# Kernel optimization log

Hardware: AMD Instinct MI355X
Metric: run time of the kernel (lower is better)

## Reference

```python
import jax, jax.numpy as jnp
import numpy as np

N_NODES = 50000
N_EDGES = 800000
IN_DIM = 128
HID = 32
HEADS = 4


def _lin_init(key, fan_in, fan_out):
    k1, k2 = jax.random.split(key)
    s = 1.0 / np.sqrt(fan_in)
    W = jax.random.uniform(k1, (fan_in, fan_out), jnp.float32, -s, s)
    b = jax.random.uniform(k2, (fan_out,), jnp.float32, -s, s)
    return W, b


def setup_inputs() -> dict:
    key = jax.random.key(0)
    keys = jax.random.split(key, 12)
    x = jax.random.normal(keys[0], (N_NODES, IN_DIM), jnp.float32)
    edge_index = jax.random.randint(keys[1], (2, N_EDGES), 0, N_NODES, jnp.int64)

    # conv1: in_dim -> heads*hid (128 -> 4*32)
    Wq1, bq1 = _lin_init(keys[2], IN_DIM, HEADS * HID)
    Wk1, bk1 = _lin_init(keys[3], IN_DIM, HEADS * HID)
    Wv1, bv1 = _lin_init(keys[4], IN_DIM, HEADS * HID)
    Ws1, bs1 = _lin_init(keys[5], IN_DIM, HEADS * HID)
    # conv2: 128 -> 1*32
    Wq2, bq2 = _lin_init(keys[6], HEADS * HID, HID)
    Wk2, bk2 = _lin_init(keys[7], HEADS * HID, HID)
    Wv2, bv2 = _lin_init(keys[8], HEADS * HID, HID)
    Ws2, bs2 = _lin_init(keys[9], HEADS * HID, HID)
    # output linear: 32 -> 1
    Wo, bo = _lin_init(keys[10], HID, 1)

    return {
        "x": x, "edge_index": edge_index,
        "Wq1": Wq1, "bq1": bq1, "Wk1": Wk1, "bk1": bk1,
        "Wv1": Wv1, "bv1": bv1, "Ws1": Ws1, "bs1": bs1,
        "Wq2": Wq2, "bq2": bq2, "Wk2": Wk2, "bk2": bk2,
        "Wv2": Wv2, "bv2": bv2, "Ws2": Ws2, "bs2": bs2,
        "Wo": Wo, "bo": bo,
    }


def transformer_conv(x, edge_index, Wq, bq, Wk, bk, Wv, bv, Ws, bs, heads, d):
    # PyG TransformerConv (concat=True, root_weight=True, beta=False, no edge attr).
    n = x.shape[0]
    src, dst = edge_index[0], edge_index[1]  # message j(src) -> i(dst)
    q = (x @ Wq + bq).reshape(n, heads, d)
    k = (x @ Wk + bk).reshape(n, heads, d)
    v = (x @ Wv + bv).reshape(n, heads, d)
    # per-edge attention logits [E, heads]
    logits = (q[dst] * k[src]).sum(-1) / jnp.sqrt(jnp.float32(d))
    # segment softmax over incoming edges of each target node
    m = jax.ops.segment_max(logits, dst, num_segments=n)
    p = jnp.exp(logits - m[dst])
    denom = jax.ops.segment_sum(p, dst, num_segments=n)
    alpha = p / denom[dst]  # [E, heads]
    # weighted scatter-add of values
    msg = alpha[:, :, None] * v[src]  # [E, heads, d]
    aggr = jax.ops.segment_sum(msg, dst, num_segments=n).reshape(n, heads * d)
    return aggr + x @ Ws + bs  # root (skip) connection


def reference(x, edge_index,
              Wq1, bq1, Wk1, bk1, Wv1, bv1, Ws1, bs1,
              Wq2, bq2, Wk2, bk2, Wv2, bv2, Ws2, bs2,
              Wo, bo):
    h = transformer_conv(x, edge_index, Wq1, bq1, Wk1, bk1, Wv1, bv1, Ws1, bs1, HEADS, HID)
    h = jax.nn.relu(h)
    h = transformer_conv(h, edge_index, Wq2, bq2, Wk2, bk2, Wv2, bv2, Ws2, bs2, 1, HID)
    h = jax.nn.relu(h)
    g = h.mean(axis=0)  # [HID]
    return g @ Wo + bo  # [1]
```

## Files before the change

kernel.cpp:

```cpp
#include <hip/hip_runtime.h>
#include <math.h>

#define N_NODES 50000
#define N_EDGES 800000
#define NBK 196
#define BCAP 6144

typedef short short8 __attribute__((ext_vector_type(8)));
typedef float f32x4 __attribute__((ext_vector_type(4)));
typedef float f32x2 __attribute__((ext_vector_type(2)));

__device__ inline unsigned short f2bf(float v) {
  unsigned u = __float_as_uint(v);
  u += 0x7FFFu + ((u >> 16) & 1u);
  return (unsigned short)(u >> 16);
}
__device__ inline float bf2f(unsigned short b) {
  return __uint_as_float(((unsigned)b) << 16);
}
__device__ inline float bflo(unsigned u) { return __uint_as_float(u << 16); }
__device__ inline float bfhi(unsigned u) { return __uint_as_float(u & 0xFFFF0000u); }
__device__ inline unsigned char f2fp8(float v) {
  return (unsigned char)(__builtin_amdgcn_cvt_pk_fp8_f32(v, 0.f, 0, false) & 0xFF);
}
template <bool HI>
__device__ inline f32x2 fp8dec(unsigned u) {
  return __builtin_amdgcn_cvt_pk_f32_fp8(u, HI);
}

#define SCL 0.17677669529663687f

#define W1_B 256
#define W2_B 64
__global__ void prep_fused(const float* __restrict__ Wq1, const float* __restrict__ Wk1,
                           const float* __restrict__ Wv1, const float* __restrict__ Ws1,
                           const float* __restrict__ bq1, const float* __restrict__ bk1,
                           const float* __restrict__ bv1, const float* __restrict__ bs1,
                           const float* __restrict__ Wq2, const float* __restrict__ Wk2,
                           const float* __restrict__ Wv2, const float* __restrict__ Ws2,
                           const float* __restrict__ bq2, const float* __restrict__ bk2,
                           const float* __restrict__ bv2, const float* __restrict__ bs2,
                           unsigned short* __restrict__ Wt1, float* __restrict__ bcat1,
                           unsigned short* __restrict__ Wt2, float* __restrict__ bcat2,
                           const int* __restrict__ ei, int* __restrict__ bhist, int E) {
  const int b = blockIdx.x, tid = threadIdx.x;
  if (b < W1_B) {
    int i = b * 256 + tid;
    int c = i >> 7, k = i & 127;
    int mi = c >> 7, lc = c & 127;
    const float* W = (mi == 0) ? Wq1 : (mi == 1) ? Wk1 : (mi == 2) ? Wv1 : Ws1;
    float scl = (mi == 0) ? SCL : 1.f;
    Wt1[i] = f2bf(W[(size_t)k * 128 + lc] * scl);
    if (i < 512) {
      int bm = i >> 7, bl = i & 127;
      const float* bb = (bm == 0) ? bq1 : (bm == 1) ? bk1 : (bm == 2) ? bv1 : bs1;
      bcat1[i] = bb[bl] * ((bm == 0) ? SCL : 1.f);
    }
  } else if (b < W1_B + W2_B) {
    int i = (b - W1_B) * 256 + tid;
    int c = i >> 7, k = i & 127;
    int mi = c >> 5, lc = c & 31;
    const float* W = (mi == 0) ? Wq2 : (mi == 1) ? Wk2 : (mi == 2) ? Wv2 : Ws2;
    float scl = (mi == 0) ? SCL : 1.f;
    Wt2[i] = f2bf(W[(size_t)k * 32 + lc] * scl);
    if (i < 128) {
      int bm = i >> 5, bl = i & 31;
      const float* bb = (bm == 0) ? bq2 : (bm == 1) ? bk2 : (bm == 2) ? bv2 : bs2;
      bcat2[i] = bb[bl] * ((bm == 0) ? SCL : 1.f);
    }
  } else {
    __shared__ int h[NBK];
    for (int i = tid; i < NBK; i += 256) h[i] = 0;
    __syncthreads();
    int e = (b - W1_B - W2_B) * 4096 + tid;
#pragma unroll
    for (int p = 0; p < 16; ++p, e += 256)
      if (e < E) atomicAdd(&h[ei[E + e] >> 8], 1);
    __syncthreads();
    for (int i = tid; i < NBK; i += 256)
      if (h[i]) atomicAdd(&bhist[i], h[i]);
  }
}

__global__ __launch_bounds__(256) void gemm_conv1(
    const float* __restrict__ X, const unsigned short* __restrict__ Wt,
    const float* __restrict__ bcat, unsigned short* __restrict__ Q1b,
    unsigned short* __restrict__ SK1, unsigned char* __restrict__ KV8, int M) {
  __shared__ __align__(16) unsigned char L[3][64 * 272];
  unsigned short* As = (unsigned short*)L[0];
  const int bm = blockIdx.x * 64;
  const int tid = threadIdx.x, wave = tid >> 6, lane = tid & 63;
  const int lr = lane & 15, q = lane >> 4;

#pragma unroll
  for (int p = 0; p < 8; ++p) {
    int f = tid + p * 256;
    int row = f >> 5, c4 = f & 31;
    int gm = bm + row; if (gm >= M) gm = 0;
    float4 v = *(const float4*)(X + (size_t)gm * 128 + c4 * 4);
    ushort4 o;
    o.x = f2bf(v.x); o.y = f2bf(v.y); o.z = f2bf(v.z); o.w = f2bf(v.w);
    *(ushort4*)&As[row * 136 + c4 * 4] = o;
  }
  __syncthreads();

  const int colbase = wave * 128;
  f32x4 acc[4][8];
#pragma unroll
  for (int i = 0; i < 4; ++i)
#pragma unroll
    for (int j = 0; j < 8; ++j) acc[i][j] = (f32x4){0.f, 0.f, 0.f, 0.f};

#pragma unroll
  for (int ks = 0; ks < 4; ++ks) {
    short8 af[4];
#pragma unroll
    for (int i = 0; i < 4; ++i)
      af[i] = *(short8*)&As[(i * 16 + lr) * 136 + ks * 32 + q * 8];
#pragma unroll
    for (int j = 0; j < 8; ++j) {
      short8 bf = *(const short8*)(Wt + (size_t)(colbase + j * 16 + lr) * 128 + ks * 32 + q * 8);
#pragma unroll
      for (int i = 0; i < 4; ++i)
        acc[i][j] = __builtin_amdgcn_mfma_f32_16x16x32_bf16(af[i], bf, acc[i][j], 0, 0, 0);
    }
  }
  __syncthreads();

  float bj[8];
#pragma unroll
  for (int j = 0; j < 8; ++j) bj[j] = bcat[colbase + j * 16 + lr];

  if (wave == 0 || wave == 3) {
    unsigned short* Ls16 = (unsigned short*)((wave == 0) ? L[1] : L[0]);
#pragma unroll
    for (int i = 0; i < 4; ++i)
#pragma unroll
      for (int r = 0; r < 4; ++r) {
        int row = i * 16 + q * 4 + r;
#pragma unroll
        for (int j = 0; j < 8; ++j)
          Ls16[row * 136 + j * 16 + lr] = f2bf(acc[i][j][r] + bj[j]);
      }
  } else {
    unsigned char* KLs = L[2];
    const int voff = (wave == 2) ? 2 : 0;
#pragma unroll
    for (int i = 0; i < 4; ++i)
#pragma unroll
      for (int r = 0; r < 4; ++r) {
        int row = i * 16 + q * 4 + r;
#pragma unroll
        for (int j = 0; j < 8; ++j) {
          int d = j * 16 + lr;
          KLs[row * 272 + 4 * (d >> 1) + voff + (d & 1)] = f2fp8(acc[i][j][r] + bj[j]);
        }
      }
  }
  __syncthreads();

#pragma unroll
  for (int p = 0; p < 4; ++p) {
    int f = tid + p * 256;
    int row = f >> 4, u = f & 15;
    int gr = bm + row;
    if (gr < M) {
      *(uint4*)(Q1b + (size_t)gr * 128 + u * 8) = *(uint4*)&((unsigned short*)L[1])[row * 136 + u * 8];
      *(uint4*)(KV8 + (size_t)gr * 256 + u * 16) = *(uint4*)&L[2][row * 272 + u * 16];
      *(uint4*)(SK1 + (size_t)gr * 128 + u * 8) = *(uint4*)&((unsigned short*)L[0])[row * 136 + u * 8];
    }
  }
}

__global__ __launch_bounds__(256) void gemm2(
    const unsigned short* __restrict__ Ab, const unsigned short* __restrict__ Wt,
    const float* __restrict__ bcat, unsigned char* __restrict__ C2b, int M) {
  __shared__ __align__(16) unsigned short As[64 * 136];
  __shared__ __align__(16) unsigned char Lsb[64 * 272];
  const int bm = blockIdx.x * 64;
  const int tid = threadIdx.x, wave = tid >> 6, lane = tid & 63;
  const int lr = lane & 15, q = lane >> 4;

#pragma unroll
  for (int p = 0; p < 4; ++p) {
    int f = tid + p * 256;
    int row = f >> 4, chunk = f & 15;
    int gm = bm + row; if (gm >= M) gm = 0;
    uint4 v = *(const uint4*)(Ab + (size_t)gm * 128 + chunk * 8);
    *(uint4*)&As[row * 136 + chunk * 8] = v;
  }
  __syncthreads();

  f32x4 acc[4][2];
#pragma unroll
  for (int i = 0; i < 4; ++i)
#pragma unroll
    for (int j = 0; j < 2; ++j) acc[i][j] = (f32x4){0.f, 0.f, 0.f, 0.f};

#pragma unroll
  for (int ks = 0; ks < 4; ++ks) {
    short8 af[4];
#pragma unroll
    for (int i = 0; i < 4; ++i)
      af[i] = *(short8*)&As[(i * 16 + lr) * 136 + ks * 32 + q * 8];
#pragma unroll
    for (int j = 0; j < 2; ++j) {
      short8 bf = *(const short8*)(Wt + (size_t)(wave * 32 + j * 16 + lr) * 128 + ks * 32 + q * 8);
#pragma unroll
      for (int i = 0; i < 4; ++i)
        acc[i][j] = __builtin_amdgcn_mfma_f32_16x16x32_bf16(af[i], bf, acc[i][j], 0, 0, 0);
    }
  }

  float bj[2];
#pragma unroll
  for (int j = 0; j < 2; ++j) bj[j] = bcat[wave * 32 + j * 16 + lr];
#pragma unroll
  for (int i = 0; i < 4; ++i)
#pragma unroll
    for (int r = 0; r < 4; ++r) {
      int row = i * 16 + q * 4 + r;
#pragma unroll
      for (int j = 0; j < 2; ++j) {
        int c = wave * 32 + j * 16 + lr;
        float val = acc[i][j][r] + bj[j];
        if (c < 32) {
          *(unsigned short*)&Lsb[row * 272 + 2 * c] = f2bf(val);
        } else if (c < 64) {
          int d = c - 32;
          Lsb[row * 272 + 64 + 4 * (d >> 1) + (d & 1)] = f2fp8(val);
        } else if (c < 96) {
          int d = c - 64;
          Lsb[row * 272 + 64 + 4 * (d >> 1) + 2 + (d & 1)] = f2fp8(val);
        } else {
          *(unsigned short*)&Lsb[row * 272 + 192 + 2 * (c - 96)] = f2bf(val);
        }
      }
    }
  __syncthreads();
#pragma unroll
  for (int p = 0; p < 16; ++p) {
    int idx = tid + p * 256;
    int row = idx >> 6, u = idx & 63;
    int gr = bm + row;
    if (gr < M) *(unsigned*)(C2b + (size_t)gr * 256 + u * 4) = *(const unsigned*)&Lsb[row * 272 + u * 4];
  }
}

__global__ void bucket_scan(const int* __restrict__ bhist, int* __restrict__ boff,
                            int* __restrict__ bcur) {
  __shared__ int s[256];
  int t = threadIdx.x;
  int v = (t < NBK) ? bhist[t] : 0;
  s[t] = v;
  __syncthreads();
#pragma unroll
  for (int off = 1; off < 256; off <<= 1) {
    int u = (t >= off) ? s[t - off] : 0;
    __syncthreads();
    s[t] += u;
    __syncthreads();
  }
  if (t < NBK) {
    int excl = s[t] - v;
    boff[t] = excl;
    bcur[t] = excl;
  }
  if (t == NBK - 1) boff[NBK] = s[t];
}

__global__ void bucket_scatter(const int* __restrict__ ei, int* __restrict__ bcur,
                               int* __restrict__ ebuck, int E) {
  __shared__ int lh[NBK];
  for (int i = threadIdx.x; i < NBK; i += 256) lh[i] = 0;
  __syncthreads();
  const int e0 = blockIdx.x * 4096;
  int pks[16], bks[16];
#pragma unroll
  for (int p = 0; p < 16; ++p) {
    int e = e0 + p * 256 + threadIdx.x;
    if (e < E) {
      int src = ei[e], dst = ei[E + e];
      pks[p] = (src << 8) | (dst & 255);
      bks[p] = dst >> 8;
      atomicAdd(&lh[bks[p]], 1);
    } else bks[p] = -1;
  }
  __syncthreads();
  for (int i = threadIdx.x; i < NBK; i += 256)
    if (lh[i]) lh[i] = atomicAdd(&bcur[i], lh[i]);
  __syncthreads();
#pragma unroll
  for (int p = 0; p < 16; ++p) {
    if (bks[p] >= 0) {
      int slot = atomicAdd(&lh[bks[p]], 1);
      ebuck[slot] = pks[p];
    }
  }
}

__global__ void bucket_csr(const int* __restrict__ ebuck, const int* __restrict__ boff,
                           int* __restrict__ rowptr, int* __restrict__ esrc, int N) {
  const int b = blockIdx.x;
  const int lo = boff[b], hi = boff[b + 1];
  const int cnt = hi - lo;
  __shared__ int hist[256];
  __shared__ int cur[256];
  __shared__ int sorted[BCAP];
  const int t = threadIdx.x;
  hist[t] = 0;
  __syncthreads();
  for (int i = t; i < cnt; i += 256) atomicAdd(&hist[ebuck[lo + i] & 255], 1);
  __syncthreads();
  int v = hist[t];
  sorted[t] = v;
  __syncthreads();
#pragma unroll
  for (int off = 1; off < 256; off <<= 1) {
    int u = (t >= off) ? sorted[t - off] : 0;
    __syncthreads();
    sorted[t] += u;
    __syncthreads();
  }
  int excl = sorted[t] - v;
  cur[t] = excl;
  int node = b * 256 + t;
  if (node <= N) rowptr[node] = lo + excl;
  __syncthreads();
  for (int i = t; i < cnt; i += 256) {
    int pk = ebuck[lo + i];
    int slot = atomicAdd(&cur[pk & 255], 1);
    if (slot < BCAP) sorted[slot] = pk;
    else esrc[lo + slot] = pk & 0xFFFFFF00;
  }
  __syncthreads();
  int lim = cnt < BCAP ? cnt : BCAP;
  for (int i = t; i < lim; i += 256) esrc[lo + i] = sorted[i] & 0xFFFFFF00;
}

__global__ void node_attn1(const int* __restrict__ rowptr, const int* __restrict__ esrc,
                           const unsigned short* __restrict__ Qb,
                           const unsigned char* __restrict__ KV8,
                           const unsigned short* __restrict__ SK, unsigned short* __restrict__ Hb,
                           int n) {
  int node = (blockIdx.x * blockDim.x + threadIdx.x) >> 6;
  int lane = threadIdx.x & 63;
  if (node >= n) return;
  const int half = lane >> 5, ll = lane & 31;
  const int r0 = rowptr[node], r1 = rowptr[node + 1];
  uint2 qq = *(const uint2*)(Qb + (size_t)node * 128 + ll * 4);
  const float q0 = bflo(qq.x), q1 = bfhi(qq.x), q2 = bflo(qq.y), q3 = bfhi(qq.y);
  float l = 0.f, a0 = 0.f, a1 = 0.f, a2 = 0.f, a3 = 0.f;
  const unsigned char* kvb = KV8 + ll * 8;
  int j = r0;
  for (; j + 8 <= r1; j += 8) {
    int e = j + half * 4;
    int s0 = esrc[e], s1 = esrc[e + 1], s2 = esrc[e + 2], s3 = esrc[e + 3];
    uint2 u0 = *(const uint2*)(kvb + s0);
    uint2 u1 = *(const uint2*)(kvb + s1);
    uint2 u2 = *(const uint2*)(kvb + s2);
    uint2 u3 = *(const uint2*)(kvb + s3);
    f32x2 k0a = fp8dec<false>(u0.x), k0b = fp8dec<false>(u0.y);
    f32x2 k1a = fp8dec<false>(u1.x), k1b = fp8dec<false>(u1.y);
    f32x2 k2a = fp8dec<false>(u2.x), k2b = fp8dec<false>(u2.y);
    f32x2 k3a = fp8dec<false>(u3.x), k3b = fp8dec<false>(u3.y);
    float d0 = q0 * k0a.x + q1 * k0a.y + q2 * k0b.x + q3 * k0b.y;
    float d1 = q0 * k1a.x + q1 * k1a.y + q2 * k1b.x + q3 * k1b.y;
    float d2 = q0 * k2a.x + q1 * k2a.y + q2 * k2b.x + q3 * k2b.y;
    float d3 = q0 * k3a.x + q1 * k3a.y + q2 * k3b.x + q3 * k3b.y;
#pragma unroll
    for (int msk = 1; msk <= 4; msk <<= 1) {
      d0 += __shfl_xor(d0, msk);
      d1 += __shfl_xor(d1, msk);
      d2 += __shfl_xor(d2, msk);
      d3 += __shfl_xor(d3, msk);
    }
    float p0 = __expf(d0), p1 = __expf(d1), p2 = __expf(d2), p3 = __expf(d3);
    l += (p0 + p1) + (p2 + p3);
    f32x2 v0a = fp8dec<true>(u0.x), v0b = fp8dec<true>(u0.y);
    f32x2 v1a = fp8dec<true>(u1.x), v1b = fp8dec<true>(u1.y);
    f32x2 v2a = fp8dec<true>(u2.x), v2b = fp8dec<true>(u2.y);
    f32x2 v3a = fp8dec<true>(u3.x), v3b = fp8dec<true>(u3.y);
    a0 += p0 * v0a.x + p1 * v1a.x + p2 * v2a.x + p3 * v3a.x;
    a1 += p0 * v0a.y + p1 * v1a.y + p2 * v2a.y + p3 * v3a.y;
    a2 += p0 * v0b.x + p1 * v1b.x + p2 * v2b.x + p3 * v3b.x;
    a3 += p0 * v0b.y + p1 * v1b.y + p2 * v2b.y + p3 * v3b.y;
  }
  for (; j < r1; j += 4) {
    int eA = j + half * 2, eB = eA + 1;
    bool vA = eA < r1, vB = eB < r1;
    int sA = esrc[vA ? eA : r0];
    int sB = esrc[vB ? eB : r0];
    uint2 ua = *(const uint2*)(kvb + sA);
    uint2 ub = *(const uint2*)(kvb + sB);
    f32x2 ka1 = fp8dec<false>(ua.x), ka2 = fp8dec<false>(ua.y);
    f32x2 kb1 = fp8dec<false>(ub.x), kb2 = fp8dec<false>(ub.y);
    float dA = q0 * ka1.x + q1 * ka1.y + q2 * ka2.x + q3 * ka2.y;
    float dB = q0 * kb1.x + q1 * kb1.y + q2 * kb2.x + q3 * kb2.y;
#pragma unroll
    for (int msk = 1; msk <= 4; msk <<= 1) {
      dA += __shfl_xor(dA, msk);
      dB += __shfl_xor(dB, msk);
    }
    float pA = vA ? __expf(dA) : 0.f;
    float pB = vB ? __expf(dB) : 0.f;
    l += pA + pB;
    f32x2 va1 = fp8dec<true>(ua.x), va2 = fp8dec<true>(ua.y);
    f32x2 vb1 = fp8dec<true>(ub.x), vb2 = fp8dec<true>(ub.y);
    a0 += pA * va1.x + pB * vb1.x;
    a1 += pA * va1.y + pB * vb1.y;
    a2 += pA * va2.x + pB * vb2.x;
    a3 += pA * va2.y + pB * vb2.y;
  }
  l  += __shfl_xor(l, 32);
  a0 += __shfl_xor(a0, 32);
  a1 += __shfl_xor(a1, 32);
  a2 += __shfl_xor(a2, 32);
  a3 += __shfl_xor(a3, 32);
  float inv = (l > 0.f) ? 1.f / l : 0.f;
  if (half == 0) {
    uint2 sk = *(const uint2*)(SK + (size_t)node * 128 + ll * 4);
    float o0 = fmaxf(bflo(sk.x) + a0 * inv, 0.f);
    float o1 = fmaxf(bfhi(sk.x) + a1 * inv, 0.f);
    float o2 = fmaxf(bflo(sk.y) + a2 * inv, 0.f);
    float o3 = fmaxf(bfhi(sk.y) + a3 * inv, 0.f);
    uint2 hb;
    hb.x = ((unsigned)f2bf(o1) << 16) | (unsigned)f2bf(o0);
    hb.y = ((unsigned)f2bf(o3) << 16) | (unsigned)f2bf(o2);
    *(uint2*)(Hb + (size_t)node * 128 + ll * 4) = hb;
  }
}

__global__ void node_attn2(const int* __restrict__ rowptr, const int* __restrict__ esrc,
                           unsigned char* __restrict__ C2b, int n) {
  int node = (blockIdx.x * blockDim.x + threadIdx.x) >> 6;
  int lane = threadIdx.x & 63;
  if (node >= n) return;
  const int g = lane >> 4, gl = lane & 15;
  const int r0 = rowptr[node], r1 = rowptr[node + 1];
  unsigned qu = *(const unsigned*)(C2b + (size_t)node * 256 + gl * 4);
  const float q0 = bflo(qu), q1 = bfhi(qu);
  float l = 0.f, a0 = 0.f, a1 = 0.f;
  const unsigned char* kvb = C2b + 64 + gl * 4;
  int j = r0;
  for (; j + 8 <= r1; j += 8) {
    int e = j + g * 2;
    int s0 = esrc[e], s1 = esrc[e + 1];
    unsigned u0 = *(const unsigned*)(kvb + s0);
    unsigned u1 = *(const unsigned*)(kvb + s1);
    f32x2 k0 = fp8dec<false>(u0), k1 = fp8dec<false>(u1);
    float d0 = q0 * k0.x + q1 * k0.y;
    float d1 = q0 * k1.x + q1 * k1.y;
#pragma unroll
    for (int msk = 1; msk <= 8; msk <<= 1) {
      d0 += __shfl_xor(d0, msk);
      d1 += __shfl_xor(d1, msk);
    }
    float p0 = __expf(d0), p1 = __expf(d1);
    l += p0 + p1;
    f32x2 v0 = fp8dec<true>(u0), v1 = fp8dec<true>(u1);
    a0 += p0 * v0.x + p1 * v1.x;
    a1 += p0 * v0.y + p1 * v1.y;
  }
  for (; j < r1; j += 4) {
    bool v = (j + g) < r1;
    int s = esrc[v ? j + g : r0];
    unsigned u = *(const unsigned*)(kvb + s);
    f32x2 kd = fp8dec<false>(u);
    float d = q0 * kd.x + q1 * kd.y;
#pragma unroll
    for (int msk = 1; msk <= 8; msk <<= 1) d += __shfl_xor(d, msk);
    float p = v ? __expf(d) : 0.f;
    l += p;
    f32x2 vd = fp8dec<true>(u);
    a0 += p * vd.x;
    a1 += p * vd.y;
  }
#pragma unroll
  for (int msk = 16; msk <= 32; msk <<= 1) {
    l  += __shfl_xor(l, msk);
    a0 += __shfl_xor(a0, msk);
    a1 += __shfl_xor(a1, msk);
  }
  float inv = (l > 0.f) ? 1.f / l : 0.f;
  if (lane < 16) {
    unsigned* h = (unsigned*)(C2b + (size_t)node * 256 + 192 + gl * 4);
    unsigned hu = *h;
    float o0 = bflo(hu) + a0 * inv;
    float o1 = bfhi(hu) + a1 * inv;
    *h = ((unsigned)f2bf(o1) << 16) | (unsigned)f2bf(o0);
  }
}

__global__ void mean_reduce(const unsigned char* __restrict__ C2b, float* __restrict__ ACC, int n) {
  __shared__ float s[256];
  float acc = 0.f;
  int stride = gridDim.x * blockDim.x;
  int total = n * 32;
  for (int i = blockIdx.x * blockDim.x + threadIdx.x; i < total; i += stride) {
    int node = i >> 5, c = i & 31;
    unsigned short h = *(const unsigned short*)(C2b + (size_t)node * 256 + 192 + c * 2);
    acc += fmaxf(bf2f(h), 0.f);
  }
  s[threadIdx.x] = acc;
  __syncthreads();
  for (int off = 128; off >= 32; off >>= 1) {
    if (threadIdx.x < off) s[threadIdx.x] += s[threadIdx.x + off];
    __syncthreads();
  }
  if (threadIdx.x < 32) atomicAdd(&ACC[threadIdx.x], s[threadIdx.x]);
}

__global__ void final_out(const float* __restrict__ ACC, const float* __restrict__ Wo,
                          const float* __restrict__ bo, float* __restrict__ out, float invN) {
  int lane = threadIdx.x;
  float v = 0.f;
  if (lane < 32) v = ACC[lane] * invN * Wo[lane];
  v += __shfl_xor(v, 1);
  v += __shfl_xor(v, 2);
  v += __shfl_xor(v, 4);
  v += __shfl_xor(v, 8);
  v += __shfl_xor(v, 16);
  v += __shfl_xor(v, 32);
  if (lane == 0) out[0] = v + bo[0];
}

extern "C" void kernel_launch(void* const* d_in, const int* in_sizes, int n_in,
                              void* d_out, int out_size, void* d_ws, size_t ws_size,
                              hipStream_t stream) {
  const float* x   = (const float*)d_in[0];
  const int*   ei  = (const int*)d_in[1];
  const float* Wq1 = (const float*)d_in[2];  const float* bq1 = (const float*)d_in[3];
  const float* Wk1 = (const float*)d_in[4];  const float* bk1 = (const float*)d_in[5];
  const float* Wv1 = (const float*)d_in[6];  const float* bv1 = (const float*)d_in[7];
  const float* Ws1 = (const float*)d_in[8];  const float* bs1 = (const float*)d_in[9];
  const float* Wq2 = (const float*)d_in[10]; const float* bq2 = (const float*)d_in[11];
  const float* Wk2 = (const float*)d_in[12]; const float* bk2 = (const float*)d_in[13];
  const float* Wv2 = (const float*)d_in[14]; const float* bv2 = (const float*)d_in[15];
  const float* Ws2 = (const float*)d_in[16]; const float* bs2 = (const float*)d_in[17];
  const float* Wo  = (const float*)d_in[18]; const float* bo  = (const float*)d_in[19];

  char* ws = (char*)d_ws;
  const int N = N_NODES, E = N_EDGES;
  const int GB = (N + 63) / 64;
  const int EB = (E + 4095) / 4096;

  unsigned short* Q1b = (unsigned short*)(ws + 0);
  unsigned short* SK1 = (unsigned short*)(ws + 12800000);
  unsigned char*  KV1 = (unsigned char*)(ws + 25600000);
  unsigned short* H1b = (unsigned short*)(ws + 51200000);
  unsigned char*  C2  = (unsigned char*)(ws + 64000000);
  int* rowptr = (int*)(ws + 89600000);
  int* esrc   = (int*)(ws + 89900032);
  int* bhist  = (int*)(ws + 93100032);
  int* boff   = (int*)(ws + 93101056);
  int* bcur   = (int*)(ws + 93102080);
  unsigned short* Wt1   = (unsigned short*)(ws + 93103104);
  unsigned short* Wt2   = (unsigned short*)(ws + 93234176);
  float*          bcat1 = (float*)(ws + 93266944);
  float*          bcat2 = (float*)(ws + 93268992);
  float*          ACC   = (float*)(ws + 93269504);
  int*            ebuck = (int*)(ws + 93270016);

  float* out = (float*)d_out;

  dim3 blk(256);

  hipMemsetAsync(bhist, 0, NBK * sizeof(int), stream);
  hipMemsetAsync(ACC, 0, 32 * sizeof(float), stream);

  prep_fused<<<dim3(W1_B + W2_B + EB), blk, 0, stream>>>(
      Wq1, Wk1, Wv1, Ws1, bq1, bk1, bv1, bs1,
      Wq2, Wk2, Wv2, Ws2, bq2, bk2, bv2, bs2,
      Wt1, bcat1, Wt2, bcat2, ei, bhist, E);

  bucket_scan<<<dim3(1), blk, 0, stream>>>(bhist, boff, bcur);
  bucket_scatter<<<dim3(EB), blk, 0, stream>>>(ei, bcur, ebuck, E);
  bucket_csr<<<dim3(NBK), blk, 0, stream>>>(ebuck, boff, rowptr, esrc, N);

  gemm_conv1<<<dim3(GB), blk, 0, stream>>>(x, Wt1, bcat1, Q1b, SK1, KV1, N);

  node_attn1<<<dim3((N * 64 + 255) / 256), blk, 0, stream>>>(rowptr, esrc, Q1b, KV1, SK1, H1b, N);

  gemm2<<<dim3(GB), blk, 0, stream>>>(H1b, Wt2, bcat2, C2, N);

  node_attn2<<<dim3((N * 64 + 255) / 256), blk, 0, stream>>>(rowptr, esrc, C2, N);

  mean_reduce<<<dim3(1024), blk, 0, stream>>>(C2, ACC, N);
  final_out<<<dim3(1), dim3(64), 0, stream>>>(ACC, Wo, bo, out, 1.0f / (float)N);
}
```

Measured before the change: 270.0 us.

## Fuse edge bucket scatter into conv1 GEMM and fold mean/output into attn2

The bucket scatter blocks become a prefix of the conv1 GEMM launch, so edge bucketing and the first projection share one grid instead of running back to back. node_attn2 now applies ReLU, dots with Wo and writes one partial sum per block. A single-block final_out reduces these partials, which removes the mean_reduce kernel, the ACC memset, the global atomics and the write-back of h2. The cost is a larger fused kernel whose scatter blocks hold the same large shared-memory footprint as the GEMM blocks.

```diff
diff --git a/kernel.cpp b/kernel.cpp
--- a/kernel.cpp
+++ b/kernel.cpp
@@ -82,14 +82,69 @@
   }
 }
 
-__global__ __launch_bounds__(256) void gemm_conv1(
+__global__ void bucket_scan(const int* __restrict__ bhist, int* __restrict__ boff,
+                            int* __restrict__ bcur) {
+  __shared__ int s[256];
+  int t = threadIdx.x;
+  int v = (t < NBK) ? bhist[t] : 0;
+  s[t] = v;
+  __syncthreads();
+#pragma unroll
+  for (int off = 1; off < 256; off <<= 1) {
+    int u = (t >= off) ? s[t - off] : 0;
+    __syncthreads();
+    s[t] += u;
+    __syncthreads();
+  }
+  if (t < NBK) {
+    int excl = s[t] - v;
+    boff[t] = excl;
+    bcur[t] = excl;
+  }
+  if (t == NBK - 1) boff[NBK] = s[t];
+}
+
+__global__ __launch_bounds__(256) void scatter_gemm1(
+    const int* __restrict__ ei, int* __restrict__ bcur, int* __restrict__ ebuck, int E, int EB,
     const float* __restrict__ X, const unsigned short* __restrict__ Wt,
     const float* __restrict__ bcat, unsigned short* __restrict__ Q1b,
     unsigned short* __restrict__ SK1, unsigned char* __restrict__ KV8, int M) {
   __shared__ __align__(16) unsigned char L[3][64 * 272];
+  const int tid = threadIdx.x;
+
+  if ((int)blockIdx.x < EB) {
+    int* lh = (int*)L[0];
+    for (int i = tid; i < NBK; i += 256) lh[i] = 0;
+    __syncthreads();
+    const int e0 = blockIdx.x * 4096;
+    int pks[16], bks[16];
+#pragma unroll
+    for (int p = 0; p < 16; ++p) {
+      int e = e0 + p * 256 + tid;
+      if (e < E) {
+        int src = ei[e], dst = ei[E + e];
+        pks[p] = (src << 8) | (dst & 255);
+        bks[p] = dst >> 8;
+        atomicAdd(&lh[bks[p]], 1);
+      } else bks[p] = -1;
+    }
+    __syncthreads();
+    for (int i = tid; i < NBK; i += 256)
+      if (lh[i]) lh[i] = atomicAdd(&bcur[i], lh[i]);
+    __syncthreads();
+#pragma unroll
+    for (int p = 0; p < 16; ++p) {
+      if (bks[p] >= 0) {
+        int slot = atomicAdd(&lh[bks[p]], 1);
+        ebuck[slot] = pks[p];
+      }
+    }
+    return;
+  }
+
   unsigned short* As = (unsigned short*)L[0];
-  const int bm = blockIdx.x * 64;
-  const int tid = threadIdx.x, wave = tid >> 6, lane = tid & 63;
+  const int bm = (blockIdx.x - EB) * 64;
+  const int wave = tid >> 6, lane = tid & 63;
   const int lr = lane & 15, q = lane >> 4;
 
 #pragma unroll
@@ -170,6 +225,45 @@
       *(uint4*)(SK1 + (size_t)gr * 128 + u * 8) = *(uint4*)&((unsigned short*)L[0])[row * 136 + u * 8];
     }
   }
+}
+
+__global__ void bucket_csr(const int* __restrict__ ebuck, const int* __restrict__ boff,
+                           int* __restrict__ rowptr, int* __restrict__ esrc, int N) {
+  const int b = blockIdx.x;
+  const int lo = boff[b], hi = boff[b + 1];
+  const int cnt = hi - lo;
+  __shared__ int hist[256];
+  __shared__ int cur[256];
+  __shared__ int sorted[BCAP];
+  const int t = threadIdx.x;
+  hist[t] = 0;
+  __syncthreads();
+  for (int i = t; i < cnt; i += 256) atomicAdd(&hist[ebuck[lo + i] & 255], 1);
+  __syncthreads();
+  int v = hist[t];
+  sorted[t] = v;
+  __syncthreads();
+#pragma unroll
+  for (int off = 1; off < 256; off <<= 1) {
+    int u = (t >= off) ? sorted[t - off] : 0;
+    __syncthreads();
+    sorted[t] += u;
+    __syncthreads();
+  }
+  int excl = sorted[t] - v;
+  cur[t] = excl;
+  int node = b * 256 + t;
+  if (node <= N) rowptr[node] = lo + excl;
+  __syncthreads();
+  for (int i = t; i < cnt; i += 256) {
+    int pk = ebuck[lo + i];
+    int slot = atomicAdd(&cur[pk & 255], 1);
+    if (slot < BCAP) sorted[slot] = pk;
+    else esrc[lo + slot] = pk & 0xFFFFFF00;
+  }
+  __syncthreads();
+  int lim = cnt < BCAP ? cnt : BCAP;
+  for (int i = t; i < lim; i += 256) esrc[lo + i] = sorted[i] & 0xFFFFFF00;
 }
 
 __global__ __launch_bounds__(256) void gemm2(
@@ -245,97 +339,6 @@
     int gr = bm + row;
     if (gr < M) *(unsigned*)(C2b + (size_t)gr * 256 + u * 4) = *(const unsigned*)&Lsb[row * 272 + u * 4];
   }
-}
-
-__global__ void bucket_scan(const int* __restrict__ bhist, int* __restrict__ boff,
-                            int* __restrict__ bcur) {
-  __shared__ int s[256];
-  int t = threadIdx.x;
-  int v = (t < NBK) ? bhist[t] : 0;
-  s[t] = v;
-  __syncthreads();
-#pragma unroll
-  for (int off = 1; off < 256; off <<= 1) {
-    int u = (t >= off) ? s[t - off] : 0;
-    __syncthreads();
-    s[t] += u;
-    __syncthreads();
-  }
-  if (t < NBK) {
-    int excl = s[t] - v;
-    boff[t] = excl;
-    bcur[t] = excl;
-  }
-  if (t == NBK - 1) boff[NBK] = s[t];
-}
-
-__global__ void bucket_scatter(const int* __restrict__ ei, int* __restrict__ bcur,
-                               int* __restrict__ ebuck, int E) {
-  __shared__ int lh[NBK];
-  for (int i = threadIdx.x; i < NBK; i += 256) lh[i] = 0;
-  __syncthreads();
-  const int e0 = blockIdx.x * 4096;
-  int pks[16], bks[16];
-#pragma unroll
-  for (int p = 0; p < 16; ++p) {
-    int e = e0 + p * 256 + threadIdx.x;
-    if (e < E) {
-      int src = ei[e], dst = ei[E + e];
-      pks[p] = (src << 8) | (dst & 255);
-      bks[p] = dst >> 8;
-      atomicAdd(&lh[bks[p]], 1);
-    } else bks[p] = -1;
-  }
-  __syncthreads();
-  for (int i = threadIdx.x; i < NBK; i += 256)
-    if (lh[i]) lh[i] = atomicAdd(&bcur[i], lh[i]);
-  __syncthreads();
-#pragma unroll
-  for (int p = 0; p < 16; ++p) {
-    if (bks[p] >= 0) {
-      int slot = atomicAdd(&lh[bks[p]], 1);
-      ebuck[slot] = pks[p];
-    }
-  }
-}
-
-__global__ void bucket_csr(const int* __restrict__ ebuck, const int* __restrict__ boff,
-                           int* __restrict__ rowptr, int* __restrict__ esrc, int N) {
-  const int b = blockIdx.x;
-  const int lo = boff[b], hi = boff[b + 1];
-  const int cnt = hi - lo;
-  __shared__ int hist[256];
-  __shared__ int cur[256];
-  __shared__ int sorted[BCAP];
-  const int t = threadIdx.x;
-  hist[t] = 0;
-  __syncthreads();
-  for (int i = t; i < cnt; i += 256) atomicAdd(&hist[ebuck[lo + i] & 255], 1);
-  __syncthreads();
-  int v = hist[t];
-  sorted[t] = v;
-  __syncthreads();
-#pragma unroll
-  for (int off = 1; off < 256; off <<= 1) {
-    int u = (t >= off) ? sorted[t - off] : 0;
-    __syncthreads();
-    sorted[t] += u;
-    __syncthreads();
-  }
-  int excl = sorted[t] - v;
-  cur[t] = excl;
-  int node = b * 256 + t;
-  if (node <= N) rowptr[node] = lo + excl;
-  __syncthreads();
-  for (int i = t; i < cnt; i += 256) {
-    int pk = ebuck[lo + i];
-    int slot = atomicAdd(&cur[pk & 255], 1);
-    if (slot < BCAP) sorted[slot] = pk;
-    else esrc[lo + slot] = pk & 0xFFFFFF00;
-  }
-  __syncthreads();
-  int lim = cnt < BCAP ? cnt : BCAP;
-  for (int i = t; i < lim; i += 256) esrc[lo + i] = sorted[i] & 0xFFFFFF00;
 }
 
 __global__ void node_attn1(const int* __restrict__ rowptr, const int* __restrict__ esrc,
@@ -432,97 +435,85 @@
 }
 
 __global__ void node_attn2(const int* __restrict__ rowptr, const int* __restrict__ esrc,
-                           unsigned char* __restrict__ C2b, int n) {
+                           const unsigned char* __restrict__ C2b, const float* __restrict__ Wo,
+                           float* __restrict__ pblock, int n) {
+  __shared__ float ps[4];
   int node = (blockIdx.x * blockDim.x + threadIdx.x) >> 6;
   int lane = threadIdx.x & 63;
-  if (node >= n) return;
+  int wave = threadIdx.x >> 6;
   const int g = lane >> 4, gl = lane & 15;
-  const int r0 = rowptr[node], r1 = rowptr[node + 1];
-  unsigned qu = *(const unsigned*)(C2b + (size_t)node * 256 + gl * 4);
-  const float q0 = bflo(qu), q1 = bfhi(qu);
-  float l = 0.f, a0 = 0.f, a1 = 0.f;
-  const unsigned char* kvb = C2b + 64 + gl * 4;
-  int j = r0;
-  for (; j + 8 <= r1; j += 8) {
-    int e = j + g * 2;
-    int s0 = esrc[e], s1 = esrc[e + 1];
-    unsigned u0 = *(const unsigned*)(kvb + s0);
-    unsigned u1 = *(const unsigned*)(kvb + s1);
-    f32x2 k0 = fp8dec<false>(u0), k1 = fp8dec<false>(u1);
-    float d0 = q0 * k0.x + q1 * k0.y;
-    float d1 = q0 * k1.x + q1 * k1.y;
-#pragma unroll
-    for (int msk = 1; msk <= 8; msk <<= 1) {
-      d0 += __shfl_xor(d0, msk);
-      d1 += __shfl_xor(d1, msk);
-    }
-    float p0 = __expf(d0), p1 = __expf(d1);
-    l += p0 + p1;
-    f32x2 v0 = fp8dec<true>(u0), v1 = fp8dec<true>(u1);
-    a0 += p0 * v0.x + p1 * v1.x;
-    a1 += p0 * v0.y + p1 * v1.y;
-  }
-  for (; j < r1; j += 4) {
-    bool v = (j + g) < r1;
-    int s = esrc[v ? j + g : r0];
-    unsigned u = *(const unsigned*)(kvb + s);
-    f32x2 kd = fp8dec<false>(u);
-    float d = q0 * kd.x + q1 * kd.y;
-#pragma unroll
-    for (int msk = 1; msk <= 8; msk <<= 1) d += __shfl_xor(d, msk);
-    float p = v ? __expf(d) : 0.f;
-    l += p;
-    f32x2 vd = fp8dec<true>(u);
-    a0 += p * vd.x;
-    a1 += p * vd.y;
-  }
-#pragma unroll
-  for (int msk = 16; msk <= 32; msk <<= 1) {
-    l  += __shfl_xor(l, msk);
-    a0 += __shfl_xor(a0, msk);
-    a1 += __shfl_xor(a1, msk);
-  }
-  float inv = (l > 0.f) ? 1.f / l : 0.f;
-  if (lane < 16) {
-    unsigned* h = (unsigned*)(C2b + (size_t)node * 256 + 192 + gl * 4);
-    unsigned hu = *h;
-    float o0 = bflo(hu) + a0 * inv;
-    float o1 = bfhi(hu) + a1 * inv;
-    *h = ((unsigned)f2bf(o1) << 16) | (unsigned)f2bf(o0);
-  }
-}
-
-__global__ void mean_reduce(const unsigned char* __restrict__ C2b, float* __restrict__ ACC, int n) {
+  float t = 0.f;
+  if (node < n) {
+    const int r0 = rowptr[node], r1 = rowptr[node + 1];
+    unsigned qu = *(const unsigned*)(C2b + (size_t)node * 256 + gl * 4);
+    const float q0 = bflo(qu), q1 = bfhi(qu);
+    float l = 0.f, a0 = 0.f, a1 = 0.f;
+    const unsigned char* kvb = C2b + 64 + gl * 4;
+    int j = r0;
+    for (; j + 8 <= r1; j += 8) {
+      int e = j + g * 2;
+      int s0 = esrc[e], s1 = esrc[e + 1];
+      unsigned u0 = *(const unsigned*)(kvb + s0);
+      unsigned u1 = *(const unsigned*)(kvb + s1);
+      f32x2 k0 = fp8dec<false>(u0), k1 = fp8dec<false>(u1);
+      float d0 = q0 * k0.x + q1 * k0.y;
+      float d1 = q0 * k1.x + q1 * k1.y;
+#pragma unroll
+      for (int msk = 1; msk <= 8; msk <<= 1) {
+        d0 += __shfl_xor(d0, msk);
+        d1 += __shfl_xor(d1, msk);
+      }
+      float p0 = __expf(d0), p1 = __expf(d1);
+      l += p0 + p1;
+      f32x2 v0 = fp8dec<true>(u0), v1 = fp8dec<true>(u1);
+      a0 += p0 * v0.x + p1 * v1.x;
+      a1 += p0 * v0.y + p1 * v1.y;
+    }
+    for (; j < r1; j += 4) {
+      bool v = (j + g) < r1;
+      int s = esrc[v ? j + g : r0];
+      unsigned u = *(const unsigned*)(kvb + s);
+      f32x2 kd = fp8dec<false>(u);
+      float d = q0 * kd.x + q1 * kd.y;
+#pragma unroll
+      for (int msk = 1; msk <= 8; msk <<= 1) d += __shfl_xor(d, msk);
+      float p = v ? __expf(d) : 0.f;
+      l += p;
+      f32x2 vd = fp8dec<true>(u);
+      a0 += p * vd.x;
+      a1 += p * vd.y;
+    }
+#pragma unroll
+    for (int msk = 16; msk <= 32; msk <<= 1) {
+      l  += __shfl_xor(l, msk);
+      a0 += __shfl_xor(a0, msk);
+      a1 += __shfl_xor(a1, msk);
+    }
+    float inv = (l > 0.f) ? 1.f / l : 0.f;
+    unsigned hu = *(const unsigned*)(C2b + (size_t)node * 256 + 192 + gl * 4);
+    float o0 = fmaxf(bflo(hu) + a0 * inv, 0.f);
+    float o1 = fmaxf(bfhi(hu) + a1 * inv, 0.f);
+    t = o0 * Wo[2 * gl] + o1 * Wo[2 * gl + 1];
+#pragma unroll
+    for (int msk = 1; msk <= 8; msk <<= 1) t += __shfl_xor(t, msk);
+  }
+  if (lane == 0) ps[wave] = t;
+  __syncthreads();
+  if (threadIdx.x == 0) pblock[blockIdx.x] = ps[0] + ps[1] + ps[2] + ps[3];
+}
+
+__global__ void final_out(const float* __restrict__ pblock, const float* __restrict__ bo,
+                          float* __restrict__ out, int nb, float invN) {
   __shared__ float s[256];
   float acc = 0.f;
-  int stride = gridDim.x * blockDim.x;
-  int total = n * 32;
-  for (int i = blockIdx.x * blockDim.x + threadIdx.x; i < total; i += stride) {
-    int node = i >> 5, c = i & 31;
-    unsigned short h = *(const unsigned short*)(C2b + (size_t)node * 256 + 192 + c * 2);
-    acc += fmaxf(bf2f(h), 0.f);
-  }
+  for (int i = threadIdx.x; i < nb; i += 256) acc += pblock[i];
   s[threadIdx.x] = acc;
   __syncthreads();
-  for (int off = 128; off >= 32; off >>= 1) {
+  for (int off = 128; off >= 1; off >>= 1) {
     if (threadIdx.x < off) s[threadIdx.x] += s[threadIdx.x + off];
     __syncthreads();
   }
-  if (threadIdx.x < 32) atomicAdd(&ACC[threadIdx.x], s[threadIdx.x]);
-}
-
-__global__ void final_out(const float* __restrict__ ACC, const float* __restrict__ Wo,
-                          const float* __restrict__ bo, float* __restrict__ out, float invN) {
-  int lane = threadIdx.x;
-  float v = 0.f;
-  if (lane < 32) v = ACC[lane] * invN * Wo[lane];
-  v += __shfl_xor(v, 1);
-  v += __shfl_xor(v, 2);
-  v += __shfl_xor(v, 4);
-  v += __shfl_xor(v, 8);
-  v += __shfl_xor(v, 16);
-  v += __shfl_xor(v, 32);
-  if (lane == 0) out[0] = v + bo[0];
+  if (threadIdx.x == 0) out[0] = s[0] * invN + bo[0];
 }
 
 extern "C" void kernel_launch(void* const* d_in, const int* in_sizes, int n_in,
@@ -544,6 +535,7 @@
   const int N = N_NODES, E = N_EDGES;
   const int GB = (N + 63) / 64;
   const int EB = (E + 4095) / 4096;
+  const int AB = (N * 64) / 256;
 
   unsigned short* Q1b = (unsigned short*)(ws + 0);
   unsigned short* SK1 = (unsigned short*)(ws + 12800000);
@@ -559,15 +551,14 @@
   unsigned short* Wt2   = (unsigned short*)(ws + 93234176);
   float*          bcat1 = (float*)(ws + 93266944);
   float*          bcat2 = (float*)(ws + 93268992);
-  float*          ACC   = (float*)(ws + 93269504);
-  int*            ebuck = (int*)(ws + 93270016);
+  float*          pblock = (float*)(ws + 93269504);
+  int*            ebuck = (int*)(ws + 93319552);
 
   float* out = (float*)d_out;
 
   dim3 blk(256);
 
   hipMemsetAsync(bhist, 0, NBK * sizeof(int), stream);
-  hipMemsetAsync(ACC, 0, 32 * sizeof(float), stream);
 
   prep_fused<<<dim3(W1_B + W2_B + EB), blk, 0, stream>>>(
       Wq1, Wk1, Wv1, Ws1, bq1, bk1, bv1, bs1,
@@ -575,17 +566,17 @@
       Wt1, bcat1, Wt2, bcat2, ei, bhist, E);
 
   bucket_scan<<<dim3(1), blk, 0, stream>>>(bhist, boff, bcur);
-  bucket_scatter<<<dim3(EB), blk, 0, stream>>>(ei, bcur, ebuck, E);
+
+  scatter_gemm1<<<dim3(EB + GB), blk, 0, stream>>>(
+      ei, bcur, ebuck, E, EB, x, Wt1, bcat1, Q1b, SK1, KV1, N);
+
   bucket_csr<<<dim3(NBK), blk, 0, stream>>>(ebuck, boff, rowptr, esrc, N);
 
-  gemm_conv1<<<dim3(GB), blk, 0, stream>>>(x, Wt1, bcat1, Q1b, SK1, KV1, N);
-
-  node_attn1<<<dim3((N * 64 + 255) / 256), blk, 0, stream>>>(rowptr, esrc, Q1b, KV1, SK1, H1b, N);
+  node_attn1<<<dim3(AB), blk, 0, stream>>>(rowptr, esrc, Q1b, KV1, SK1, H1b, N);
 
   gemm2<<<dim3(GB), blk, 0, stream>>>(H1b, Wt2, bcat2, C2, N);
 
-  node_attn2<<<dim3((N * 64 + 255) / 256), blk, 0, stream>>>(rowptr, esrc, C2, N);
-
-  mean_reduce<<<dim3(1024), blk, 0, stream>>>(C2, ACC, N);
-  final_out<<<dim3(1), dim3(64), 0, stream>>>(ACC, Wo, bo, out, 1.0f / (float)N);
-}
+  node_attn2<<<dim3(AB), blk, 0, stream>>>(rowptr, esrc, C2, Wo, pblock, N);
+
+  final_out<<<dim3(1), blk, 0, stream>>>(pblock, bo, out, AB, 1.0f / (float)N);
+}
```

New measurement: 249.9 us, median of 2. 7.4% less time.
